# Optimization experiments

Hardware: AMD Instinct MI355X
Metric: run time of the kernel (lower is better)

## Reference

```python
import jax, jax.numpy as jnp
import numpy as np

B, C, N = 8, 128, 4096
C2 = C // 2
BN_EPS = 1e-5


def setup_inputs() -> dict:
    key = jax.random.key(0)
    ks = jax.random.split(key, 8)
    s = 1.0 / np.sqrt(C)
    s2 = 1.0 / np.sqrt(C2)
    return {
        "x": jax.random.normal(ks[0], (B, C, N), dtype=jnp.float32),
        "w_qk": jax.random.uniform(ks[1], (C2, C), jnp.float32, -s, s),  # shared q/k weight
        "w_v": jax.random.uniform(ks[2], (C2, C), jnp.float32, -s, s),
        "b_v": jax.random.uniform(ks[3], (C2,), jnp.float32, -s, s),
        "w_x": jax.random.uniform(ks[4], (C2, C), jnp.float32, -s, s),
        "w_t": jax.random.uniform(ks[5], (C2, C2), jnp.float32, -s2, s2),
        "b_t": jax.random.uniform(ks[6], (C2,), jnp.float32, -s2, s2),
        "gamma": jnp.ones((C2,), jnp.float32),
        "beta": jnp.zeros((C2,), jnp.float32),
    }


def reference(x, w_qk, w_v, b_v, w_x, w_t, b_t, gamma, beta):
    # 1x1 convs are per-point linear maps: [B,C,N] -> [B,C2,N]
    x_q = jnp.einsum("oc,bcn->bno", w_qk, x)          # [B, N, C2]
    x_k = jnp.einsum("oc,bcn->bon", w_qk, x)          # [B, C2, N]
    x_v = jnp.einsum("oc,bcn->bon", w_v, x) + b_v[None, :, None]

    energy = jnp.einsum("bno,bom->bnm", x_q, x_k)     # [B, N, N]
    attn = jax.nn.softmax(energy, axis=-1)            # row softmax
    attn = attn / (1e-9 + attn.sum(axis=1, keepdims=True))  # column L1 renorm

    x_r = jnp.einsum("bon,bnm->bom", x_v, attn)       # [B, C2, N]
    x_c = jnp.einsum("oc,bcn->bon", w_x, x)           # [B, C2, N]

    d = x_c - x_r
    t = jnp.einsum("oi,bin->bon", w_t, d) + b_t[None, :, None]
    # BatchNorm1d (training-mode batch stats) over (B, N) per channel
    mean = t.mean(axis=(0, 2), keepdims=True)
    var = t.var(axis=(0, 2), keepdims=True)
    t_hat = (t - mean) * jax.lax.rsqrt(var + BN_EPS)
    x_r2 = jax.nn.relu(gamma[None, :, None] * t_hat + beta[None, :, None])
    return x_c + x_r2
```

## Files before the change

### kernel.cpp

```cpp
#include <hip/hip_runtime.h>

#define B_   8
#define C_   128
#define N_   4096
#define C2_  64

typedef __bf16 bf16x8 __attribute__((ext_vector_type(8)));
typedef float  f32x4  __attribute__((ext_vector_type(4)));

#define MFMA16(a, b, c) __builtin_amdgcn_mfma_f32_16x16x32_bf16((a), (b), (c), 0, 0, 0)

#define QK_SCALE 1.2011224087864498f

static __device__ __forceinline__ unsigned short f2bf(float f) {
    union { __bf16 b; unsigned short u; } cv;
    cv.b = (__bf16)f;
    return cv.u;
}
static __device__ __forceinline__ float bf2f(unsigned short u) {
    union { unsigned int u; float f; } cv;
    cv.u = ((unsigned int)u) << 16;
    return cv.f;
}

struct us4 { unsigned short a, b, c, d; };

static __device__ __forceinline__ void gl_lds16(const unsigned short* g, void* l) {
    __builtin_amdgcn_global_load_lds(
        (const __attribute__((address_space(1))) unsigned int*)g,
        (__attribute__((address_space(3))) unsigned int*)l,
        16, 0, 0);
}

__global__ __launch_bounds__(256) void k1_proj(
    const float* __restrict__ x, const float* __restrict__ w_qk,
    const float* __restrict__ w_v, const float* __restrict__ b_v,
    const float* __restrict__ w_x,
    unsigned short* __restrict__ qk_t, unsigned short* __restrict__ xv_bf,
    float* __restrict__ xc)
{
    __shared__ __align__(16) unsigned short w_lds[192 * 136];
    __shared__ __align__(16) unsigned short x_t[64 * 136];
    const int tid = threadIdx.x;
    const int wave = tid >> 6, lane = tid & 63;
    const int quad = lane >> 4, col = lane & 15;
    const int b = blockIdx.y;
    const int n0 = blockIdx.x * 64;

    const float* wsrc[3] = {w_qk, w_v, w_x};
    #pragma unroll
    for (int mat = 0; mat < 3; ++mat) {
        const float* wm = wsrc[mat];
        #pragma unroll
        for (int it = 0; it < 8; ++it) {
            const int idx = it * 256 + tid;
            const int o = idx >> 5, c = (idx & 31) * 4;
            const float4 v = *(const float4*)(wm + o * C_ + c);
            us4 pk;
            pk.a = f2bf(v.x); pk.b = f2bf(v.y); pk.c = f2bf(v.z); pk.d = f2bf(v.w);
            *(us4*)&w_lds[(mat * 64 + o) * 136 + c] = pk;
        }
    }
    const float* xb = x + (size_t)b * C_ * N_ + n0;
    #pragma unroll
    for (int it = 0; it < 8; ++it) {
        const int idx = it * 256 + tid;
        const int c = idx >> 4, n = (idx & 15) * 4;
        const float4 v = *(const float4*)(xb + (size_t)c * N_ + n);
        x_t[(n + 0) * 136 + c] = f2bf(v.x);
        x_t[(n + 1) * 136 + c] = f2bf(v.y);
        x_t[(n + 2) * 136 + c] = f2bf(v.z);
        x_t[(n + 3) * 136 + c] = f2bf(v.w);
    }
    __syncthreads();

    const int nw = wave * 16;
    bf16x8 bfr[4];
    #pragma unroll
    for (int kt = 0; kt < 4; ++kt)
        bfr[kt] = *(const bf16x8*)&x_t[(nw + col) * 136 + kt * 32 + quad * 8];

    const int n_g = n0 + nw + col;

    #pragma unroll
    for (int ot = 0; ot < 12; ++ot) {
        f32x4 acc = {0.f, 0.f, 0.f, 0.f};
        #pragma unroll
        for (int kt = 0; kt < 4; ++kt) {
            const bf16x8 afr = *(const bf16x8*)&w_lds[(ot * 16 + col) * 136 + kt * 32 + quad * 8];
            acc = MFMA16(afr, bfr[kt], acc);
        }
        if (ot < 4) {
            us4 pk;
            pk.a = f2bf(acc[0] * QK_SCALE); pk.b = f2bf(acc[1] * QK_SCALE);
            pk.c = f2bf(acc[2] * QK_SCALE); pk.d = f2bf(acc[3] * QK_SCALE);
            *(us4*)&qk_t[(size_t)(b * N_ + n_g) * C2_ + ot * 16 + quad * 4] = pk;
        } else if (ot < 8) {
            const float4 bv4 = *(const float4*)(b_v + (ot - 4) * 16 + quad * 4);
            const float* bvp = (const float*)&bv4;
            #pragma unroll
            for (int r = 0; r < 4; ++r)
                xv_bf[(size_t)(b * C2_ + (ot - 4) * 16 + quad * 4 + r) * N_ + n_g]
                    = f2bf(acc[r] + bvp[r]);
        } else {
            #pragma unroll
            for (int r = 0; r < 4; ++r)
                xc[(size_t)(b * C2_ + (ot - 8) * 16 + quad * 4 + r) * N_ + n_g] = acc[r];
        }
    }
}

__global__ __launch_bounds__(256) void k2_rowstats(
    const unsigned short* __restrict__ qk_t, float* __restrict__ part_rs)
{
    __shared__ __align__(16) unsigned char lds_raw[2 * 16384];
    const int tid = threadIdx.x;
    const int wave = tid >> 6, lane = tid & 63;
    const int quad = lane >> 4, col = lane & 15;
    const int b = blockIdx.x & 7;
    const int nblk = (blockIdx.x >> 3) & 31;
    const int mq = blockIdx.x >> 8;
    const int n_base = nblk * 128 + wave * 32;
    const int m_start = mq * 512;
    const unsigned short* qb = qk_t + (size_t)b * N_ * C2_;

    bf16x8 a0[2], a1[2];
    #pragma unroll
    for (int s = 0; s < 2; ++s) {
        const unsigned short* p = qb + (size_t)(n_base + s * 16 + col) * C2_ + quad * 8;
        a0[s] = *(const bf16x8*)p;
        a1[s] = *(const bf16x8*)(p + 32);
    }

    auto stage = [&](int m0, int p) {
        unsigned char* base = lds_raw + p * 16384;
        #pragma unroll
        for (int r = 0; r < 4; ++r) {
            const int idx = r * 256 + tid;
            const int row = idx >> 3, seg = idx & 7;
            gl_lds16(qb + (size_t)(m0 + row) * C2_ + (size_t)(seg ^ (row & 7)) * 8,
                     base + idx * 16);
        }
    };

    float run_s[2][4];
    #pragma unroll
    for (int s = 0; s < 2; ++s)
        #pragma unroll
        for (int r = 0; r < 4; ++r) run_s[s][r] = 0.f;

    stage(m_start, 0);

    for (int c = 0; c < 4; ++c) {
        const int p = c & 1;
        asm volatile("s_waitcnt vmcnt(0)" ::: "memory");
        __builtin_amdgcn_s_barrier();
        asm volatile("" ::: "memory");
        if (c + 1 < 4) stage(m_start + (c + 1) * 128, 1 - p);
        const unsigned short* qt = (const unsigned short*)(lds_raw + p * 16384);
        #pragma unroll
        for (int ms = 0; ms < 8; ++ms) {
            const int row = ms * 16 + col;
            const bf16x8 b0 = *(const bf16x8*)(qt + row * 64 + ((quad ^ (col & 7)) * 8));
            const bf16x8 b1 = *(const bf16x8*)(qt + row * 64 + (((4 + quad) ^ (col & 7)) * 8));
            #pragma unroll
            for (int s = 0; s < 2; ++s) {
                f32x4 acc = {0.f, 0.f, 0.f, 0.f};
                __builtin_amdgcn_s_setprio(1);
                acc = MFMA16(a0[s], b0, acc);
                acc = MFMA16(a1[s], b1, acc);
                __builtin_amdgcn_s_setprio(0);
                #pragma unroll
                for (int r = 0; r < 4; ++r)
                    run_s[s][r] += __builtin_amdgcn_exp2f(acc[r]);
            }
        }
    }

    #pragma unroll
    for (int s = 0; s < 2; ++s)
        #pragma unroll
        for (int r = 0; r < 4; ++r) {
            #pragma unroll
            for (int off = 1; off < 16; off <<= 1)
                run_s[s][r] += __shfl_xor(run_s[s][r], off, 64);
        }
    if (col == 0) {
        #pragma unroll
        for (int s = 0; s < 2; ++s)
            #pragma unroll
            for (int r = 0; r < 4; ++r)
                part_rs[((size_t)(mq * 8 + b) << 12) + n_base + s * 16 + quad * 4 + r]
                    = run_s[s][r];
    }
}

__global__ __launch_bounds__(256) void k2bc(
    const float* __restrict__ part_rs, unsigned short* __restrict__ xv_bf,
    unsigned short* __restrict__ wbf)
{
    __shared__ float wl[64];
    const int tid = threadIdx.x;
    const int b = blockIdx.x & 7;
    const int n0 = (blockIdx.x >> 3) * 64;
    if (tid < 64) {
        float s = 0.f;
        #pragma unroll
        for (int q = 0; q < 8; ++q)
            s += part_rs[((size_t)(q * 8 + b) << 12) + n0 + tid];
        const float w = 1.0f / s;
        wl[tid] = w;
        wbf[b * N_ + n0 + tid] = f2bf(w);
    }
    __syncthreads();
    #pragma unroll
    for (int it = 0; it < 4; ++it) {
        const int idx4 = it * 256 + tid;
        const int o = idx4 >> 4, n4 = (idx4 & 15) * 4;
        unsigned short* p = xv_bf + (size_t)(b * C2_ + o) * N_ + n0 + n4;
        us4 v = *(us4*)p;
        v.a = f2bf(bf2f(v.a) * wl[n4 + 0]);
        v.b = f2bf(bf2f(v.b) * wl[n4 + 1]);
        v.c = f2bf(bf2f(v.c) * wl[n4 + 2]);
        v.d = f2bf(bf2f(v.d) * wl[n4 + 3]);
        *(us4*)p = v;
    }
}

__global__ __launch_bounds__(256, 3) void k3_pv(
    const unsigned short* __restrict__ qk_t, const unsigned short* __restrict__ xv_bf,
    const unsigned short* __restrict__ wbf,
    unsigned short* __restrict__ yb0, unsigned short* __restrict__ yb1,
    unsigned short* __restrict__ yb2, unsigned short* __restrict__ yb3,
    float* __restrict__ cspart)
{
    __shared__ __align__(16) unsigned char lds_raw[16384 + 4 * 5120];
    const int tid = threadIdx.x;
    const int wave = tid >> 6, lane = tid & 63;
    const int quad = lane >> 4, col = lane & 15;
    const int nh2 = wave & 1, mh = wave >> 1;
    const int b = blockIdx.x & 7;
    const int m_blk = ((blockIdx.x >> 3) & 31) * 128;
    const int sk = blockIdx.x >> 8;
    const int n_start = sk * 1024;
    const int m_wave = m_blk + mh * 64;
    const unsigned short* qb = qk_t + (size_t)b * N_ * C2_;
    const unsigned short* vb = xv_bf + (size_t)b * C2_ * N_;
    const unsigned short* wb = wbf + b * N_;
    unsigned short* yp = (sk == 0) ? yb0 : (sk == 1) ? yb1 : (sk == 2) ? yb2 : yb3;

    unsigned short* kbl = (unsigned short*)lds_raw;
    #pragma unroll
    for (int p = 0; p < 4; ++p) {
        const int row = p * 32 + (tid >> 3), slot = tid & 7;
        *(uint4*)(kbl + row * 64 + ((slot ^ (row & 7)) * 8)) =
            *(const uint4*)(qb + (size_t)(m_blk + row) * C2_ + slot * 8);
    }
    unsigned short* stS = (unsigned short*)(lds_raw + 16384 + wave * 5120);
    __syncthreads();

    f32x4 accY[4][4];
    #pragma unroll
    for (int g = 0; g < 4; ++g)
        #pragma unroll
        for (int os = 0; os < 4; ++os) accY[g][os] = (f32x4){0.f, 0.f, 0.f, 0.f};
    f32x4 csacc[4];
    #pragma unroll
    for (int g = 0; g < 4; ++g) csacc[g] = (f32x4){0.f, 0.f, 0.f, 0.f};

    const int sw0 = (quad ^ (col & 7)) * 8;
    const int sw1 = ((4 + quad) ^ (col & 7)) * 8;

    for (int c = 0; c < 16; ++c) {
        const int n0 = n_start + c * 64;

        const bf16x8 wfrag = *(const bf16x8*)(wb + n0 + nh2 * 32 + quad * 8);

        #pragma unroll
        for (int ns = 0; ns < 2; ++ns) {
            const int row = n0 + nh2 * 32 + ns * 16 + col;
            const bf16x8 qa0 = *(const bf16x8*)(qb + (size_t)row * C2_ + quad * 8);
            const bf16x8 qa1 = *(const bf16x8*)(qb + (size_t)row * C2_ + 32 + quad * 8);
            #pragma unroll
            for (int g = 0; g < 4; ++g) {
                const int rl = (mh * 64 + g * 16 + col) * 64;
                const bf16x8 kb0 = *(const bf16x8*)(kbl + rl + sw0);
                const bf16x8 kb1 = *(const bf16x8*)(kbl + rl + sw1);
                f32x4 acc = {0.f, 0.f, 0.f, 0.f};
                acc = MFMA16(qa0, kb0, acc);
                acc = MFMA16(qa1, kb1, acc);
                union { unsigned short us[4]; uint2 u2; } pk;
                #pragma unroll
                for (int r = 0; r < 4; ++r)
                    pk.us[r] = f2bf(__builtin_amdgcn_exp2f(acc[r]));
                *(uint2*)&stS[(g * 16 + col) * 40 + ns * 16 + quad * 4] = pk.u2;
            }
        }

        bf16x8 sB[4];
        #pragma unroll
        for (int g = 0; g < 4; ++g)
            sB[g] = *(const bf16x8*)&stS[(g * 16 + col) * 40 + quad * 8];

        #pragma unroll
        for (int g = 0; g < 4; ++g)
            csacc[g] = MFMA16(wfrag, sB[g], csacc[g]);

        #pragma unroll
        for (int os = 0; os < 4; ++os) {
            const bf16x8 va = *(const bf16x8*)(
                vb + (size_t)(os * 16 + col) * N_ + n0 + nh2 * 32 + quad * 8);
            __builtin_amdgcn_s_setprio(1);
            #pragma unroll
            for (int g = 0; g < 4; ++g)
                accY[g][os] = MFMA16(va, sB[g], accY[g][os]);
            __builtin_amdgcn_s_setprio(0);
        }
    }

    __syncthreads();
    float* cmb = (float*)lds_raw;
    float* csc = (float*)(lds_raw + 32768);
    if (nh2 == 1) {
        #pragma unroll
        for (int g = 0; g < 4; ++g) {
            #pragma unroll
            for (int os = 0; os < 4; ++os)
                #pragma unroll
                for (int r = 0; r < 4; ++r)
                    cmb[((mh * 16 + g * 4 + os) * 4 + r) * 64 + lane] = accY[g][os][r];
            csc[(mh * 4 + g) * 64 + lane] = csacc[g][0];
        }
    }
    __syncthreads();
    if (nh2 == 0) {
        #pragma unroll
        for (int g = 0; g < 4; ++g) {
            const float cs = csacc[g][0] + csc[(mh * 4 + g) * 64 + lane];
            if (lane < 16)
                cspart[((size_t)sk * 8 + b) * N_ + m_wave + g * 16 + lane] = cs;
            #pragma unroll
            for (int os = 0; os < 4; ++os)
                #pragma unroll
                for (int r = 0; r < 4; ++r) {
                    const float v = accY[g][os][r] +
                        cmb[((mh * 16 + g * 4 + os) * 4 + r) * 64 + lane];
                    yp[(size_t)(b * C2_ + os * 16 + quad * 4 + r) * N_ + m_wave + g * 16 + col]
                        = f2bf(v);
                }
        }
    }
}

__global__ __launch_bounds__(256) void k4_t(
    const float* __restrict__ xc, const unsigned short* __restrict__ y0,
    const unsigned short* __restrict__ y1, const unsigned short* __restrict__ y2,
    const unsigned short* __restrict__ y3,
    const float* __restrict__ cspart, const float* __restrict__ w_t,
    const float* __restrict__ b_t, float* __restrict__ t_buf,
    float* __restrict__ part_bn)
{
    __shared__ __align__(16) unsigned short wlds[64 * 72];
    __shared__ __align__(16) unsigned short d_t[64 * 72];
    __shared__ float cinv[64];
    const int tid = threadIdx.x;
    const int wave = tid >> 6, lane = tid & 63;
    const int quad = lane >> 4, col = lane & 15;
    const int b = blockIdx.y;
    const int n0 = blockIdx.x * 64;
    const size_t base = (size_t)b * C2_ * N_;

    #pragma unroll
    for (int it = 0; it < 4; ++it) {
        const int idx4 = it * 256 + tid;
        const int o = idx4 >> 4, i4 = (idx4 & 15) * 4;
        const float4 v = *(const float4*)(w_t + o * 64 + i4);
        us4 pk;
        pk.a = f2bf(v.x); pk.b = f2bf(v.y); pk.c = f2bf(v.z); pk.d = f2bf(v.w);
        *(us4*)&wlds[o * 72 + i4] = pk;
    }
    if (tid < 64) {
        const int n = n0 + tid;
        const float cs = cspart[(size_t)b * N_ + n] + cspart[(size_t)(8 + b) * N_ + n]
                       + cspart[(size_t)(16 + b) * N_ + n] + cspart[(size_t)(24 + b) * N_ + n];
        cinv[tid] = 1.0f / (1e-9f + cs);
    }
    __syncthreads();

    #pragma unroll
    for (int it = 0; it < 4; ++it) {
        const int idx4 = it * 256 + tid;
        const int i = idx4 >> 4, n4 = (idx4 & 15) * 4;
        const size_t g = base + (size_t)i * N_ + n0 + n4;
        const float4 c4 = *(const float4*)(xc + g);
        const us4 u0 = *(const us4*)(y0 + g);
        const us4 u1 = *(const us4*)(y1 + g);
        const us4 u2 = *(const us4*)(y2 + g);
        const us4 u3 = *(const us4*)(y3 + g);
        d_t[(n4 + 0) * 72 + i] = f2bf(c4.x - (bf2f(u0.a) + bf2f(u1.a) + bf2f(u2.a) + bf2f(u3.a)) * cinv[n4 + 0]);
        d_t[(n4 + 1) * 72 + i] = f2bf(c4.y - (bf2f(u0.b) + bf2f(u1.b) + bf2f(u2.b) + bf2f(u3.b)) * cinv[n4 + 1]);
        d_t[(n4 + 2) * 72 + i] = f2bf(c4.z - (bf2f(u0.c) + bf2f(u1.c) + bf2f(u2.c) + bf2f(u3.c)) * cinv[n4 + 2]);
        d_t[(n4 + 3) * 72 + i] = f2bf(c4.w - (bf2f(u0.d) + bf2f(u1.d) + bf2f(u2.d) + bf2f(u3.d)) * cinv[n4 + 3]);
    }
    __syncthreads();

    const int ow = wave * 16;
    bf16x8 afr[2];
    #pragma unroll
    for (int kt = 0; kt < 2; ++kt)
        afr[kt] = *(const bf16x8*)&wlds[(ow + col) * 72 + kt * 32 + quad * 8];
    const float4 bt4 = *(const float4*)(b_t + ow + quad * 4);
    const float* btp = (const float*)&bt4;

    float s[4] = {0.f, 0.f, 0.f, 0.f}, q2[4] = {0.f, 0.f, 0.f, 0.f};
    #pragma unroll
    for (int ns = 0; ns < 4; ++ns) {
        f32x4 acc = {0.f, 0.f, 0.f, 0.f};
        #pragma unroll
        for (int kt = 0; kt < 2; ++kt) {
            const bf16x8 bfr = *(const bf16x8*)&d_t[(ns * 16 + col) * 72 + kt * 32 + quad * 8];
            acc = MFMA16(afr[kt], bfr, acc);
        }
        #pragma unroll
        for (int r = 0; r < 4; ++r) {
            const float t = acc[r] + btp[r];
            t_buf[base + (size_t)(ow + quad * 4 + r) * N_ + n0 + ns * 16 + col] = t;
            s[r] += t;
            q2[r] += t * t;
        }
    }
    #pragma unroll
    for (int r = 0; r < 4; ++r) {
        #pragma unroll
        for (int off = 1; off < 16; off <<= 1) {
            s[r]  += __shfl_xor(s[r],  off, 64);
            q2[r] += __shfl_xor(q2[r], off, 64);
        }
    }
    if (col == 0) {
        const int blk = blockIdx.x * 8 + b;
        #pragma unroll
        for (int r = 0; r < 4; ++r) {
            part_bn[(size_t)(ow + quad * 4 + r) * 512 + blk]      = s[r];
            part_bn[(size_t)(64 + ow + quad * 4 + r) * 512 + blk] = q2[r];
        }
    }
}

__global__ __launch_bounds__(256) void k5r(
    const float* __restrict__ part_bn, float* __restrict__ bn)
{
    const int c = blockIdx.x;
    const int tid = threadIdx.x, wave = tid >> 6, lane = tid & 63;
    float s = 0.f;
    for (int j = tid; j < 512; j += 256) s += part_bn[(size_t)c * 512 + j];
    #pragma unroll
    for (int off = 1; off < 64; off <<= 1) s += __shfl_xor(s, off, 64);
    __shared__ float red[4];
    if (lane == 0) red[wave] = s;
    __syncthreads();
    if (tid == 0) bn[c] = red[0] + red[1] + red[2] + red[3];
}

__global__ __launch_bounds__(256) void k6_out(
    const float* __restrict__ xc, const float* __restrict__ t_buf,
    const float* __restrict__ bn, const float* __restrict__ gamma,
    const float* __restrict__ beta, float* __restrict__ out)
{
    const int idx = blockIdx.x * 256 + threadIdx.x;
    const int o = (idx >> 10) & 63;
    const float invC = 1.0f / (float)(B_ * N_);
    const float mean = bn[o] * invC;
    const float var  = bn[64 + o] * invC - mean * mean;
    const float sc = gamma[o] * rsqrtf(var + 1e-5f);
    const float sh = beta[o] - mean * sc;
    const float4 t4 = ((const float4*)t_buf)[idx];
    const float4 c4 = ((const float4*)xc)[idx];
    float4 r;
    r.x = c4.x + fmaxf(0.f, sc * t4.x + sh);
    r.y = c4.y + fmaxf(0.f, sc * t4.y + sh);
    r.z = c4.z + fmaxf(0.f, sc * t4.z + sh);
    r.w = c4.w + fmaxf(0.f, sc * t4.w + sh);
    ((float4*)out)[idx] = r;
}

extern "C" void kernel_launch(void* const* d_in, const int* in_sizes, int n_in,
                              void* d_out, int out_size, void* d_ws, size_t ws_size,
                              hipStream_t stream) {
    const float* x     = (const float*)d_in[0];
    const float* w_qk  = (const float*)d_in[1];
    const float* w_v   = (const float*)d_in[2];
    const float* b_v   = (const float*)d_in[3];
    const float* w_x   = (const float*)d_in[4];
    const float* w_t   = (const float*)d_in[5];
    const float* b_t   = (const float*)d_in[6];
    const float* gamma = (const float*)d_in[7];
    const float* beta  = (const float*)d_in[8];
    float* out = (float*)d_out;

    char* ws = (char*)d_ws;
    unsigned short* qk_t  = (unsigned short*)ws;
    unsigned short* xv_bf = (unsigned short*)(ws + (4  << 20));
    float* xc      = (float*)(ws + (8  << 20));
    unsigned short* yb0 = (unsigned short*)(ws + (16 << 20));
    unsigned short* yb1 = (unsigned short*)(ws + (20 << 20));
    float* t_buf   = (float*)(ws + (24 << 20));
    float* part_rs = (float*)(ws + (32 << 20));
    float* cspart  = (float*)(ws + (32 << 20));
    unsigned short* wbf = (unsigned short*)(ws + (33 << 20));
    float* part_bn = (float*)(ws + (33 << 20) + (64 << 10));
    float* bn      = (float*)(ws + (33 << 20) + (320 << 10));
    unsigned short* yb2 = (unsigned short*)out;
    unsigned short* yb3 = (unsigned short*)((char*)d_out + (4 << 20));

    hipLaunchKernelGGL(k1_proj,     dim3(64, 8),  256, 0, stream,
                       x, w_qk, w_v, b_v, w_x, qk_t, xv_bf, xc);
    hipLaunchKernelGGL(k2_rowstats, dim3(2048),   256, 0, stream, qk_t, part_rs);
    hipLaunchKernelGGL(k2bc,        dim3(512),    256, 0, stream, part_rs, xv_bf, wbf);
    hipLaunchKernelGGL(k3_pv,       dim3(1024),   256, 0, stream,
                       qk_t, xv_bf, wbf, yb0, yb1, yb2, yb3, cspart);
    hipLaunchKernelGGL(k4_t,        dim3(64, 8),  256, 0, stream,
                       xc, yb0, yb1, yb2, yb3, cspart, w_t, b_t, t_buf, part_bn);
    hipLaunchKernelGGL(k5r,         dim3(128),    256, 0, stream, part_bn, bn);
    hipLaunchKernelGGL(k6_out,      dim3(2048),   256, 0, stream, xc, t_buf, bn, gamma, beta, out);
}
```

Before: 192.6 us.

## Keep K fragments in registers and prefetch Q/V tiles in PV kernel

Moves each wave's K (key) fragments from a shared LDS tile into registers loaded once at kernel start, removing the LDS staging and the initial barrier. Q fragments for the next chunk are software-prefetched while the current chunk runs, and V fragments are loaded at the top of each iteration instead of just before their MFMAs. The setprio hints are dropped and launch bounds are lowered from 3 to 2 blocks per CU. This hides global load latency at the cost of more registers and lower occupancy.

```diff
diff --git a/kernel.cpp b/kernel.cpp
--- a/kernel.cpp
+++ b/kernel.cpp
@@ -227,14 +227,14 @@
     }
 }
 
-__global__ __launch_bounds__(256, 3) void k3_pv(
+__global__ __launch_bounds__(256, 2) void k3_pv(
     const unsigned short* __restrict__ qk_t, const unsigned short* __restrict__ xv_bf,
     const unsigned short* __restrict__ wbf,
     unsigned short* __restrict__ yb0, unsigned short* __restrict__ yb1,
     unsigned short* __restrict__ yb2, unsigned short* __restrict__ yb3,
     float* __restrict__ cspart)
 {
-    __shared__ __align__(16) unsigned char lds_raw[16384 + 4 * 5120];
+    __shared__ __align__(16) unsigned char lds_raw[34816];
     const int tid = threadIdx.x;
     const int wave = tid >> 6, lane = tid & 63;
     const int quad = lane >> 4, col = lane & 15;
@@ -249,15 +249,15 @@
     const unsigned short* wb = wbf + b * N_;
     unsigned short* yp = (sk == 0) ? yb0 : (sk == 1) ? yb1 : (sk == 2) ? yb2 : yb3;
 
-    unsigned short* kbl = (unsigned short*)lds_raw;
-    #pragma unroll
-    for (int p = 0; p < 4; ++p) {
-        const int row = p * 32 + (tid >> 3), slot = tid & 7;
-        *(uint4*)(kbl + row * 64 + ((slot ^ (row & 7)) * 8)) =
-            *(const uint4*)(qb + (size_t)(m_blk + row) * C2_ + slot * 8);
-    }
-    unsigned short* stS = (unsigned short*)(lds_raw + 16384 + wave * 5120);
-    __syncthreads();
+    bf16x8 kb0[4], kb1[4];
+    #pragma unroll
+    for (int g = 0; g < 4; ++g) {
+        const unsigned short* p = qb + (size_t)(m_wave + g * 16 + col) * C2_ + quad * 8;
+        kb0[g] = *(const bf16x8*)p;
+        kb1[g] = *(const bf16x8*)(p + 32);
+    }
+
+    unsigned short* stS = (unsigned short*)(lds_raw + wave * 5120);
 
     f32x4 accY[4][4];
     #pragma unroll
@@ -268,33 +268,53 @@
     #pragma unroll
     for (int g = 0; g < 4; ++g) csacc[g] = (f32x4){0.f, 0.f, 0.f, 0.f};
 
-    const int sw0 = (quad ^ (col & 7)) * 8;
-    const int sw1 = ((4 + quad) ^ (col & 7)) * 8;
+    const unsigned short* qrow = qb + (size_t)(n_start + nh2 * 32 + col) * C2_;
+
+    bf16x8 qa00 = *(const bf16x8*)(qrow + quad * 8);
+    bf16x8 qa01 = *(const bf16x8*)(qrow + 32 + quad * 8);
+    bf16x8 qa10 = *(const bf16x8*)(qrow + 16 * C2_ + quad * 8);
+    bf16x8 qa11 = *(const bf16x8*)(qrow + 16 * C2_ + 32 + quad * 8);
 
     for (int c = 0; c < 16; ++c) {
         const int n0 = n_start + c * 64;
 
+        bf16x8 va[4];
+        #pragma unroll
+        for (int os = 0; os < 4; ++os)
+            va[os] = *(const bf16x8*)(
+                vb + (size_t)(os * 16 + col) * N_ + n0 + nh2 * 32 + quad * 8);
         const bf16x8 wfrag = *(const bf16x8*)(wb + n0 + nh2 * 32 + quad * 8);
 
         #pragma unroll
-        for (int ns = 0; ns < 2; ++ns) {
-            const int row = n0 + nh2 * 32 + ns * 16 + col;
-            const bf16x8 qa0 = *(const bf16x8*)(qb + (size_t)row * C2_ + quad * 8);
-            const bf16x8 qa1 = *(const bf16x8*)(qb + (size_t)row * C2_ + 32 + quad * 8);
-            #pragma unroll
-            for (int g = 0; g < 4; ++g) {
-                const int rl = (mh * 64 + g * 16 + col) * 64;
-                const bf16x8 kb0 = *(const bf16x8*)(kbl + rl + sw0);
-                const bf16x8 kb1 = *(const bf16x8*)(kbl + rl + sw1);
-                f32x4 acc = {0.f, 0.f, 0.f, 0.f};
-                acc = MFMA16(qa0, kb0, acc);
-                acc = MFMA16(qa1, kb1, acc);
-                union { unsigned short us[4]; uint2 u2; } pk;
-                #pragma unroll
-                for (int r = 0; r < 4; ++r)
-                    pk.us[r] = f2bf(__builtin_amdgcn_exp2f(acc[r]));
-                *(uint2*)&stS[(g * 16 + col) * 40 + ns * 16 + quad * 4] = pk.u2;
-            }
+        for (int g = 0; g < 4; ++g) {
+            f32x4 acc = {0.f, 0.f, 0.f, 0.f};
+            acc = MFMA16(qa00, kb0[g], acc);
+            acc = MFMA16(qa01, kb1[g], acc);
+            union { unsigned short us[4]; uint2 u2; } pk;
+            #pragma unroll
+            for (int r = 0; r < 4; ++r)
+                pk.us[r] = f2bf(__builtin_amdgcn_exp2f(acc[r]));
+            *(uint2*)&stS[(g * 16 + col) * 40 + quad * 4] = pk.u2;
+        }
+        #pragma unroll
+        for (int g = 0; g < 4; ++g) {
+            f32x4 acc = {0.f, 0.f, 0.f, 0.f};
+            acc = MFMA16(qa10, kb0[g], acc);
+            acc = MFMA16(qa11, kb1[g], acc);
+            union { unsigned short us[4]; uint2 u2; } pk;
+            #pragma unroll
+            for (int r = 0; r < 4; ++r)
+                pk.us[r] = f2bf(__builtin_amdgcn_exp2f(acc[r]));
+            *(uint2*)&stS[(g * 16 + col) * 40 + 16 + quad * 4] = pk.u2;
+        }
+
+        {
+            const unsigned short* qn =
+                qrow + (size_t)((c < 15) ? (c + 1) * 64 : 0) * C2_;
+            qa00 = *(const bf16x8*)(qn + quad * 8);
+            qa01 = *(const bf16x8*)(qn + 32 + quad * 8);
+            qa10 = *(const bf16x8*)(qn + 16 * C2_ + quad * 8);
+            qa11 = *(const bf16x8*)(qn + 16 * C2_ + 32 + quad * 8);
         }
 
         bf16x8 sB[4];
@@ -307,15 +327,10 @@
             csacc[g] = MFMA16(wfrag, sB[g], csacc[g]);
 
         #pragma unroll
-        for (int os = 0; os < 4; ++os) {
-            const bf16x8 va = *(const bf16x8*)(
-                vb + (size_t)(os * 16 + col) * N_ + n0 + nh2 * 32 + quad * 8);
-            __builtin_amdgcn_s_setprio(1);
+        for (int os = 0; os < 4; ++os)
             #pragma unroll
             for (int g = 0; g < 4; ++g)
-                accY[g][os] = MFMA16(va, sB[g], accY[g][os]);
-            __builtin_amdgcn_s_setprio(0);
-        }
+                accY[g][os] = MFMA16(va[os], sB[g], accY[g][os]);
     }
 
     __syncthreads();
```

Measured after the change: 195.4 us. No clear change (+1.5%).
